# Optimization experiments

Hardware: AMD Instinct MI355X
Metric: run time of the kernel (lower is better)

The kernel has to match this reference:

```python
import jax, jax.numpy as jnp
import numpy as np

B, N, D, M, H = 8, 576, 512, 16, 8
DH = D // H
K = int(D * 0.1)  # sparsity_ratio=0.1 -> k=51
EPS = 1e-5


def setup_inputs() -> dict:
    key = jax.random.key(0)
    ks = jax.random.split(key, 12)
    s = 0.02
    return {
        "F_clean": jax.random.normal(ks[0], (B, N, D), jnp.float32),
        "in_proj_w": jax.random.normal(ks[1], (3 * D, D), jnp.float32) * s,
        "in_proj_b": jnp.zeros((3 * D,), jnp.float32),
        "out_proj_w": jax.random.normal(ks[2], (D, D), jnp.float32) * s,
        "out_proj_b": jnp.zeros((D,), jnp.float32),
        "w1": jax.random.normal(ks[3], (D, D), jnp.float32) * s,
        "b1": jnp.zeros((D,), jnp.float32),
        "ln_g": jnp.ones((D,), jnp.float32),
        "ln_b": jnp.zeros((D,), jnp.float32),
        "w2": jax.random.normal(ks[4], (M, D), jnp.float32) * s,
        "b2": jnp.zeros((M,), jnp.float32),
        "templates": jax.random.normal(ks[5], (M, D), jnp.float32),
    }


def reference(F_clean, in_proj_w, in_proj_b, out_proj_w, out_proj_b,
              w1, b1, ln_g, ln_b, w2, b2, templates):
    # --- self attention (torch MultiheadAttention, batch_first, eval mode) ---
    qkv = F_clean @ in_proj_w.T + in_proj_b              # [B,N,3D]
    q, k_, v = jnp.split(qkv, 3, axis=-1)
    def heads(t):
        return t.reshape(B, N, H, DH).transpose(0, 2, 1, 3)  # [B,H,N,dh]
    q, k_, v = heads(q), heads(k_), heads(v)
    scores = jnp.einsum('bhqd,bhkd->bhqk', q, k_) / jnp.sqrt(jnp.float32(DH))
    attn = jax.nn.softmax(scores, axis=-1)
    o = jnp.einsum('bhqk,bhkd->bhqd', attn, v).transpose(0, 2, 1, 3).reshape(B, N, D)
    attn_out = o @ out_proj_w.T + out_proj_b

    F_enh = F_clean + attn_out

    # --- decompose_mlp: Linear -> LayerNorm -> GELU(exact) -> Linear ---
    h = F_enh @ w1.T + b1
    mu = jnp.mean(h, axis=-1, keepdims=True)
    var = jnp.var(h, axis=-1, keepdims=True)
    h = (h - mu) / jnp.sqrt(var + EPS) * ln_g + ln_b
    h = jax.nn.gelu(h, approximate=False)
    components = h @ w2.T + b2                           # [B,N,M]

    # --- outer product: Q[b,n,d,m] = F[b,n,d] * templates[m,d] * comp[b,n,m] ---
    Q = F_clean[:, :, :, None] * templates.T[None, None, :, :] * components[:, :, None, :]

    # --- top-k sparsify along D for each (b,n,m) row ---
    Qr = Q.transpose(0, 1, 3, 2).reshape(B * N * M, D)
    _, topk_idx = jax.lax.top_k(jnp.abs(Qr), K)
    rows = jnp.arange(B * N * M)[:, None]
    mask = jnp.zeros_like(Qr).at[rows, topk_idx].set(1.0)
    Q_sparse = (Qr * mask).reshape(B, N, M, D).transpose(0, 1, 3, 2)
    return Q_sparse
```

## Files before the change

kernel.cpp:

```cpp
#include <hip/hip_runtime.h>
#include <math.h>

#define NNB   576
#define BNR   4608
#define KSEL  51

typedef unsigned short u16;
typedef __attribute__((ext_vector_type(8))) short bf16x8;
typedef __attribute__((ext_vector_type(4))) float f32x4;

__device__ __forceinline__ u16 f2bf(float f) {
    unsigned u = __float_as_uint(f);
    return (u16)((u + 0x8000u) >> 16);
}
__device__ __forceinline__ unsigned pack2(float a, float b) {
    unsigned ua = __float_as_uint(a), ub = __float_as_uint(b);
    return ((ua + 0x8000u) >> 16) | ((ub + 0x8000u) & 0xffff0000u);
}
__device__ __forceinline__ void load_lds16(const void* gp, void* lp) {
    __builtin_amdgcn_global_load_lds((const __attribute__((address_space(1))) void*)gp,
                                     (__attribute__((address_space(3))) void*)lp, 16, 0, 0);
}

__global__ __launch_bounds__(256)
void cast_bf16(const float* __restrict__ F, const float* __restrict__ ipw,
               const float* __restrict__ opw, const float* __restrict__ w1,
               u16* __restrict__ Fb, u16* __restrict__ ipwb,
               u16* __restrict__ opwb, u16* __restrict__ w1b)
{
    size_t i4 = ((size_t)blockIdx.x * 256 + threadIdx.x) * 4;
    const float* src; u16* dst; size_t off;
    if      (i4 < 2359296) { src = F;   dst = Fb;   off = i4; }
    else if (i4 < 3145728) { src = ipw; dst = ipwb; off = i4 - 2359296; }
    else if (i4 < 3407872) { src = opw; dst = opwb; off = i4 - 3145728; }
    else                   { src = w1;  dst = w1b;  off = i4 - 3407872; }
    float4 v = *(const float4*)(src + off);
    uint2 o; o.x = pack2(v.x, v.y); o.y = pack2(v.z, v.w);
    *(uint2*)(dst + off) = o;
}

template<bool RESID, bool OUT_BF16, bool QSCALE>
__global__ __launch_bounds__(256)
void gemm_mfma(const u16* __restrict__ A, const u16* __restrict__ Bw,
               const float* __restrict__ bias, const float* __restrict__ res,
               void* __restrict__ Cv, int Mr, int Nc, int Kd)
{
    __shared__ uint4 As4[1024];
    __shared__ uint4 Bs4[1024];
    const int tid = threadIdx.x;
    const int lane = tid & 63, w = tid >> 6;
    const int wu = __builtin_amdgcn_readfirstlane(w);
    const int r16 = lane & 15, quad = lane >> 4;
    const int wy = w >> 1, wx = w & 1;
    const int r0 = blockIdx.y << 7, c0 = blockIdx.x << 7;

    const u16* pA[4]; const u16* pB[4];
    #pragma unroll
    for (int rd = 0; rd < 4; ++rd) {
        const int c = (rd << 8) + tid;
        const int kb = c >> 9, g = (c >> 6) & 7, rr = (c >> 2) & 15, q = c & 3;
        const int row = (g << 4) + rr;
        const int koff = (kb << 5) + (q << 3);
        pA[rd] = A  + (size_t)(r0 + row) * Kd + koff;
        pB[rd] = Bw + (size_t)(c0 + row) * Kd + koff;
    }

    f32x4 acc[4][4];
    #pragma unroll
    for (int i = 0; i < 4; ++i)
        #pragma unroll
        for (int j = 0; j < 4; ++j) acc[i][j] = (f32x4){0.f, 0.f, 0.f, 0.f};

    for (int kk = 0; kk < Kd; kk += 64) {
        __syncthreads();
        #pragma unroll
        for (int rd = 0; rd < 4; ++rd) {
            load_lds16(pA[rd] + kk, (void*)(As4 + (rd << 8) + (wu << 6)));
            load_lds16(pB[rd] + kk, (void*)(Bs4 + (rd << 8) + (wu << 6)));
        }
        __syncthreads();
        #pragma unroll
        for (int kb = 0; kb < 2; ++kb) {
            bf16x8 af[4], bfr[4];
            #pragma unroll
            for (int i = 0; i < 4; ++i)
                af[i] = *(const bf16x8*)&As4[((kb * 8 + (wy << 2) + i) << 6) + (r16 << 2) + quad];
            #pragma unroll
            for (int j = 0; j < 4; ++j)
                bfr[j] = *(const bf16x8*)&Bs4[((kb * 8 + (wx << 2) + j) << 6) + (r16 << 2) + quad];
            #pragma unroll
            for (int i = 0; i < 4; ++i)
                #pragma unroll
                for (int j = 0; j < 4; ++j)
                    acc[i][j] = __builtin_amdgcn_mfma_f32_16x16x32_bf16(af[i], bfr[j], acc[i][j], 0, 0, 0);
        }
    }

    float bcol[4]; float scl[4];
    #pragma unroll
    for (int j = 0; j < 4; ++j) {
        const int col = c0 + (wx << 6) + (j << 4) + r16;
        bcol[j] = bias[col];
        scl[j] = (QSCALE && col < 512) ? 0.180336880111120426f : 1.0f;
    }
    #pragma unroll
    for (int i = 0; i < 4; ++i) {
        #pragma unroll
        for (int reg = 0; reg < 4; ++reg) {
            const int row = r0 + (wy << 6) + (i << 4) + (quad << 2) + reg;
            const size_t base = (size_t)row * Nc;
            #pragma unroll
            for (int j = 0; j < 4; ++j) {
                const int col = c0 + (wx << 6) + (j << 4) + r16;
                float v = acc[i][j][reg] + bcol[j];
                if (RESID) v += res[base + col];
                if (QSCALE) v *= scl[j];
                if (OUT_BF16) ((u16*)Cv)[base + col] = f2bf(v);
                else          ((float*)Cv)[base + col] = v;
            }
        }
    }
}

template<bool RESID, bool OUT_BF16>
__global__ __launch_bounds__(256)
void gemm_mfma64(const u16* __restrict__ A, const u16* __restrict__ Bw,
                 const float* __restrict__ bias, const float* __restrict__ res,
                 void* __restrict__ Cv, int Mr, int Nc, int Kd)
{
    __shared__ uint4 As4[512];
    __shared__ uint4 Bs4[1024];
    const int tid = threadIdx.x;
    const int lane = tid & 63, w = tid >> 6;
    const int wu = __builtin_amdgcn_readfirstlane(w);
    const int r16 = lane & 15, quad = lane >> 4;
    const int r0 = blockIdx.y << 6, c0 = blockIdx.x << 7;

    const u16* pA[2]; const u16* pB[4];
    #pragma unroll
    for (int rd = 0; rd < 2; ++rd) {
        const int c = (rd << 8) + tid;
        const int kb = c >> 8, g = (c >> 6) & 3, rr = (c >> 2) & 15, q = c & 3;
        pA[rd] = A + (size_t)(r0 + (g << 4) + rr) * Kd + (kb << 5) + (q << 3);
    }
    #pragma unroll
    for (int rd = 0; rd < 4; ++rd) {
        const int c = (rd << 8) + tid;
        const int kb = c >> 9, g = (c >> 6) & 7, rr = (c >> 2) & 15, q = c & 3;
        pB[rd] = Bw + (size_t)(c0 + (g << 4) + rr) * Kd + (kb << 5) + (q << 3);
    }

    f32x4 acc[4][2];
    #pragma unroll
    for (int i = 0; i < 4; ++i)
        #pragma unroll
        for (int j = 0; j < 2; ++j) acc[i][j] = (f32x4){0.f, 0.f, 0.f, 0.f};

    for (int kk = 0; kk < Kd; kk += 64) {
        __syncthreads();
        #pragma unroll
        for (int rd = 0; rd < 2; ++rd)
            load_lds16(pA[rd] + kk, (void*)(As4 + (rd << 8) + (wu << 6)));
        #pragma unroll
        for (int rd = 0; rd < 4; ++rd)
            load_lds16(pB[rd] + kk, (void*)(Bs4 + (rd << 8) + (wu << 6)));
        __syncthreads();
        #pragma unroll
        for (int kb = 0; kb < 2; ++kb) {
            bf16x8 af[4], bfr[2];
            #pragma unroll
            for (int i = 0; i < 4; ++i)
                af[i] = *(const bf16x8*)&As4[((kb * 4 + i) << 6) + (r16 << 2) + quad];
            #pragma unroll
            for (int j = 0; j < 2; ++j)
                bfr[j] = *(const bf16x8*)&Bs4[((kb * 8 + (w << 1) + j) << 6) + (r16 << 2) + quad];
            #pragma unroll
            for (int i = 0; i < 4; ++i)
                #pragma unroll
                for (int j = 0; j < 2; ++j)
                    acc[i][j] = __builtin_amdgcn_mfma_f32_16x16x32_bf16(af[i], bfr[j], acc[i][j], 0, 0, 0);
        }
    }

    float bcol[2];
    #pragma unroll
    for (int j = 0; j < 2; ++j) bcol[j] = bias[c0 + (w << 5) + (j << 4) + r16];
    #pragma unroll
    for (int i = 0; i < 4; ++i) {
        #pragma unroll
        for (int reg = 0; reg < 4; ++reg) {
            const int row = r0 + (i << 4) + (quad << 2) + reg;
            const size_t base = (size_t)row * Nc;
            #pragma unroll
            for (int j = 0; j < 2; ++j) {
                const int col = c0 + (w << 5) + (j << 4) + r16;
                float v = acc[i][j][reg] + bcol[j];
                if (RESID) v += res[base + col];
                if (OUT_BF16) ((u16*)Cv)[base + col] = f2bf(v);
                else          ((float*)Cv)[base + col] = v;
            }
        }
    }
}

__global__ __launch_bounds__(256)
void attn_mfma(const u16* __restrict__ qkv, u16* __restrict__ obuf)
{
    __shared__ uint4 Qf[512];
    __shared__ uint4 Kf[512];
    __shared__ u16  Vfs[4096];
    __shared__ u16  Pfs[4096];
    const int tid = threadIdx.x;
    const int lane = tid & 63, w = tid >> 6;
    const int wu = __builtin_amdgcn_readfirstlane(w);
    const int r16 = lane & 15, quad = lane >> 4;
    const int b = blockIdx.y >> 3, h = blockIdx.y & 7;
    const int i0 = blockIdx.x << 6;
    const u16* qb = qkv + (size_t)b * NNB * 1536 + h * 64;

    #pragma unroll
    for (int s = 0; s < 2; ++s) {
        const int linear = (s << 8) + tid;
        const int r = linear >> 3, q7 = linear & 7;
        uint4 v = *(const uint4*)(qb + (size_t)(i0 + r) * 1536 + (q7 << 3));
        Qf[(((q7 >> 2) * 4 + (r >> 4)) << 6) + ((r & 15) << 2) + (q7 & 3)] = v;
    }
    const u16* pK[2];
    #pragma unroll
    for (int rd = 0; rd < 2; ++rd) {
        const int c = (rd << 8) + tid;
        const int kb = c >> 8, g = (c >> 6) & 3, rr = (c >> 2) & 15, q = c & 3;
        pK[rd] = qb + 512 + (size_t)((g << 4) + rr) * 1536 + (kb << 5) + (q << 3);
    }

    float l_i[4] = {0.f, 0.f, 0.f, 0.f};
    f32x4 accO[4];
    #pragma unroll
    for (int f = 0; f < 4; ++f) accO[f] = (f32x4){0.f, 0.f, 0.f, 0.f};

    for (int j0 = 0; j0 < NNB; j0 += 64) {
        uint4 vR[2];
        #pragma unroll
        for (int s = 0; s < 2; ++s) {
            const int linear = (s << 8) + tid;
            const int r = linear >> 3, q7 = linear & 7;
            vR[s] = *(const uint4*)(qb + 1024 + (size_t)(j0 + r) * 1536 + (q7 << 3));
        }
        __syncthreads();
        load_lds16(pK[0] + (size_t)j0 * 1536, (void*)(Kf + (wu << 6)));
        load_lds16(pK[1] + (size_t)j0 * 1536, (void*)(Kf + 256 + (wu << 6)));
        #pragma unroll
        for (int s = 0; s < 2; ++s) {
            const int linear = (s << 8) + tid;
            const int r = linear >> 3, q7 = linear & 7;
            const u16* pe = (const u16*)&vR[s];
            const int jlow = r & 7, jq = (r >> 3) & 3, jkb = r >> 5;
            #pragma unroll
            for (int e = 0; e < 8; ++e) {
                const int d = (q7 << 3) + e;
                const int g = d >> 4;
                const int ch = ((jkb * 4 + g) << 6) + ((((d & 15) << 2) + jq) ^ g);
                Vfs[(ch << 3) + jlow] = pe[e];
            }
        }
        __syncthreads();

        f32x4 accS[4];
        #pragma unroll
        for (int f = 0; f < 4; ++f) accS[f] = (f32x4){0.f, 0.f, 0.f, 0.f};
        #pragma unroll
        for (int kb = 0; kb < 2; ++kb) {
            bf16x8 aq = *(const bf16x8*)&Qf[((kb * 4 + w) << 6) + (r16 << 2) + quad];
            #pragma unroll
            for (int f = 0; f < 4; ++f) {
                bf16x8 bk = *(const bf16x8*)&Kf[((kb * 4 + f) << 6) + (r16 << 2) + quad];
                accS[f] = __builtin_amdgcn_mfma_f32_16x16x32_bf16(aq, bk, accS[f], 0, 0, 0);
            }
        }
        #pragma unroll
        for (int reg = 0; reg < 4; ++reg) {
            const float s0 = exp2f(accS[0][reg]);
            const float s1 = exp2f(accS[1][reg]);
            const float s2 = exp2f(accS[2][reg]);
            const float s3 = exp2f(accS[3][reg]);
            l_i[reg] += (s0 + s1) + (s2 + s3);
            const int m = (quad << 2) + reg;
            const int sm = ((m & 3) << 2) + (m >> 2);
            const float pv[4] = {s0, s1, s2, s3};
            #pragma unroll
            for (int f = 0; f < 4; ++f) {
                const int k = (f << 4) + r16;
                const int ch = (((k >> 5) * 4 + w) << 6) + (((k >> 3) & 3) << 4) + sm;
                Pfs[(ch << 3) + (k & 7)] = f2bf(pv[f]);
            }
        }
        #pragma unroll
        for (int kb = 0; kb < 2; ++kb) {
            bf16x8 ap = *(const bf16x8*)&Pfs[((((kb * 4 + w) << 6) + (quad << 4) + ((r16 & 3) << 2) + (r16 >> 2)) << 3)];
            #pragma unroll
            for (int f = 0; f < 4; ++f) {
                bf16x8 bv = *(const bf16x8*)&Vfs[((((kb * 4 + f) << 6) + (((r16 << 2) + quad) ^ f)) << 3)];
                accO[f] = __builtin_amdgcn_mfma_f32_16x16x32_bf16(ap, bv, accO[f], 0, 0, 0);
            }
        }
    }
    #pragma unroll
    for (int reg = 0; reg < 4; ++reg) {
        float l = l_i[reg];
        l += __shfl_xor(l, 1); l += __shfl_xor(l, 2);
        l += __shfl_xor(l, 4); l += __shfl_xor(l, 8);
        const float inv = 1.0f / l;
        const size_t row = (size_t)(b * NNB + i0 + (w << 4) + (quad << 2) + reg);
        #pragma unroll
        for (int f = 0; f < 4; ++f)
            obuf[row * 512 + (h << 6) + (f << 4) + r16] = f2bf(accO[f][reg] * inv);
    }
}

__global__ __launch_bounds__(256)
void outer_topk(const float* __restrict__ F, const float* __restrict__ hraw,
                const float* __restrict__ lng, const float* __restrict__ lnb,
                const float* __restrict__ w2, const float* __restrict__ b2,
                const float* __restrict__ T, float* __restrict__ out)
{
    const int bn = blockIdx.x;
    const int tid = threadIdx.x;
    const int lane = tid & 63, w = tid >> 6;
    __shared__ float Fr[512];
    __shared__ float Hr[512];
    __shared__ unsigned keyslots[4][4][64];
    __shared__ float redsm[8];

    if (tid < 128)
        *(float4*)&Fr[tid << 2] = *(const float4*)(F + (size_t)bn * 512 + (tid << 2));
    const float* hp = hraw + (size_t)bn * 512;
    float x0 = hp[tid], x1 = hp[tid + 256];
    float s = x0 + x1, sq = x0 * x0 + x1 * x1;
    #pragma unroll
    for (int off = 32; off; off >>= 1) { s += __shfl_xor(s, off); sq += __shfl_xor(sq, off); }
    if (lane == 0) { redsm[w] = s; redsm[4 + w] = sq; }
    __syncthreads();
    s  = redsm[0] + redsm[1] + redsm[2] + redsm[3];
    sq = redsm[4] + redsm[5] + redsm[6] + redsm[7];
    const float mean = s * (1.0f / 512.0f);
    const float var  = sq * (1.0f / 512.0f) - mean * mean;
    const float rstd = rsqrtf(var + 1e-5f);
    float y = (x0 - mean) * rstd * lng[tid] + lnb[tid];
    Hr[tid] = 0.5f * y * (1.0f + erff(y * 0.70710678118654752f));
    y = (x1 - mean) * rstd * lng[tid + 256] + lnb[tid + 256];
    Hr[tid + 256] = 0.5f * y * (1.0f + erff(y * 0.70710678118654752f));
    __syncthreads();

    const int m0 = w << 2;
    float cm[4];
    #pragma unroll
    for (int mi = 0; mi < 4; ++mi) {
        const float* w2p = w2 + (size_t)(m0 + mi) * 512;
        float p = 0.f;
        #pragma unroll
        for (int t = 0; t < 8; ++t) p += Hr[lane + (t << 6)] * w2p[lane + (t << 6)];
        #pragma unroll
        for (int off = 32; off; off >>= 1) p += __shfl_xor(p, off);
        cm[mi] = p + b2[m0 + mi];
    }

    unsigned u[4][8]; unsigned smask[4];
    #pragma unroll
    for (int mi = 0; mi < 4; ++mi) {
        smask[mi] = 0u;
        const float* Tp = T + (size_t)(m0 + mi) * 512;
        #pragma unroll
        for (int t = 0; t < 8; ++t) {
            float pp = Fr[lane + (t << 6)] * Tp[lane + (t << 6)];
            float pc = pp * cm[mi];
            const unsigned bits = __float_as_uint(pc);
            u[mi][t] = bits & 0x7fffffffu;
            smask[mi] |= (bits >> 31) << t;
        }
    }

    unsigned pref[4] = {0u, 0u, 0u, 0u};
    int cntP[4] = {512, 512, 512, 512};
    int U[4] = {0, 0, 0, 0};
    for (int bit = 30; bit >= 23; --bit) {
        const unsigned msk = 1u << bit;
        #pragma unroll
        for (int mi = 0; mi < 4; ++mi) {
            const unsigned cand = pref[mi] | msk;
            int cnt = 0;
            #pragma unroll
            for (int t = 0; t < 8; ++t) cnt += __popcll(__ballot(u[mi][t] >= cand));
            if (cnt >= KSEL) { pref[mi] = cand; cntP[mi] = cnt; } else { U[mi] = cnt; }
        }
    }
    int blo[4];
    #pragma unroll
    for (int mi = 0; mi < 4; ++mi) {
        int b = 23;
        while ((cntP[mi] - U[mi]) > 64 && b > 0) {
            --b;
            const unsigned cand = pref[mi] | (1u << b);
            int cnt = 0;
            #pragma unroll
            for (int t = 0; t < 8; ++t) cnt += __popcll(__ballot(u[mi][t] >= cand));
            if (cnt >= KSEL) { pref[mi] = cand; cntP[mi] = cnt; } else { U[mi] = cnt; }
        }
        blo[mi] = b;
    }
    int need[4]; bool done[4];
    #pragma unroll
    for (int mi = 0; mi < 4; ++mi) {
        need[mi] = KSEL - U[mi];
        done[mi] = (need[mi] == cntP[mi] - U[mi]);
    }

    const unsigned long long lmask = (1ull << lane) - 1ull;
    unsigned kv[4] = {0u, 0u, 0u, 0u};
    #pragma unroll
    for (int mi = 0; mi < 4; ++mi) {
        if (done[mi]) continue;
        keyslots[w][mi][lane] = 0u;
        const int bl = blo[mi];
        const unsigned lowmask = (1u << bl) - 1u;
        int running = 0;
        #pragma unroll
        for (int t = 0; t < 8; ++t) {
            const bool tie = ((u[mi][t] ^ pref[mi]) >> bl) == 0u;
            const unsigned long long M = __ballot(tie);
            const int slot = running + __popcll(M & lmask);
            if (tie && slot < 64) {
                const unsigned key = ((u[mi][t] & lowmask) << 9) | (unsigned)(511 - ((t << 6) + lane));
                keyslots[w][mi][slot] = key;
            }
            running += __popcll(M);
        }
        kv[mi] = keyslots[w][mi][lane];
    }

    unsigned prefk[4] = {0u, 0u, 0u, 0u};
    for (int bb = 31; bb >= 0; --bb) {
        if (done[0] & done[1] & done[2] & done[3]) break;
        #pragma unroll
        for (int mi = 0; mi < 4; ++mi) {
            if (done[mi]) continue;
            const unsigned candk = prefk[mi] | (1u << bb);
            const int c = __popcll(__ballot(kv[mi] >= candk));
            if (c >= need[mi]) {
                prefk[mi] = candk;
                if (c == need[mi]) done[mi] = true;
            }
        }
    }

    float* ob = out + (size_t)bn * 8192 + m0;
    #pragma unroll
    for (int t = 0; t < 8; ++t) {
        const int d = (t << 6) + lane;
        float4 v;
        float* vv = &v.x;
        #pragma unroll
        for (int mi = 0; mi < 4; ++mi) {
            const unsigned uu = u[mi][t];
            const int bl = blo[mi];
            const bool tie = ((uu ^ pref[mi]) >> bl) == 0u;
            const unsigned key = ((uu & ((1u << bl) - 1u)) << 9) | (unsigned)(511 - d);
            const bool sel = (uu >= pref[mi] + (1u << bl)) || (tie && key >= prefk[mi]);
            const unsigned bits = uu | (((smask[mi] >> t) & 1u) << 31);
            vv[mi] = sel ? __uint_as_float(bits) : 0.0f;
        }
        *(float4*)(ob + (size_t)d * 16) = v;
    }
}

extern "C" void kernel_launch(void* const* d_in, const int* in_sizes, int n_in,
                              void* d_out, int out_size, void* d_ws, size_t ws_size,
                              hipStream_t stream)
{
    const float* F    = (const float*)d_in[0];
    const float* ipw  = (const float*)d_in[1];
    const float* ipb  = (const float*)d_in[2];
    const float* opw  = (const float*)d_in[3];
    const float* opb  = (const float*)d_in[4];
    const float* w1   = (const float*)d_in[5];
    const float* b1   = (const float*)d_in[6];
    const float* lng  = (const float*)d_in[7];
    const float* lnb  = (const float*)d_in[8];
    const float* w2   = (const float*)d_in[9];
    const float* b2   = (const float*)d_in[10];
    const float* tmpl = (const float*)d_in[11];

    char* wsb = (char*)d_ws;
    u16*   qkvb  = (u16*)wsb;
    u16*   obufb = (u16*)(wsb + 14155776);
    u16*   fenhb = (u16*)(wsb + 18874368);
    float* hbuf  = (float*)(wsb + 23592960);
    u16*   Fbf   = (u16*)(wsb + 33030144);
    u16*   ipwbf = (u16*)(wsb + 37748736);
    u16*   opwbf = (u16*)(wsb + 39321600);
    u16*   w1bf  = (u16*)(wsb + 39845888);

    cast_bf16<<<3584, 256, 0, stream>>>(F, ipw, opw, w1, Fbf, ipwbf, opwbf, w1bf);
    gemm_mfma<false, true, true><<<dim3(12, 36), 256, 0, stream>>>(Fbf, ipwbf, ipb, nullptr, qkvb, BNR, 1536, 512);
    attn_mfma<<<dim3(9, 64), 256, 0, stream>>>(qkvb, obufb);
    gemm_mfma64<true, true><<<dim3(4, 72), 256, 0, stream>>>(obufb, opwbf, opb, F, fenhb, BNR, 512, 512);
    gemm_mfma64<false, false><<<dim3(4, 72), 256, 0, stream>>>(fenhb, w1bf, b1, nullptr, hbuf, BNR, 512, 512);
    outer_topk<<<4608, 256, 0, stream>>>(F, hbuf, lng, lnb, w2, b2, tmpl, (float*)d_out);
}
```

Measured before the change: 296.0 us.

## Shrink GEMM tiles, pack V transposes, and use DPP reductions in top-k

The QKV projection moves from 128x128 to 64x128 tiles. The out-proj and w1 GEMMs use a new 64x64 tile kernel, which doubles the grid for better CU occupancy on the 4608-row problem. Attention V staging now loads two adjacent rows per thread and writes packed 32-bit pairs to LDS, halving LDS store count. In outer_topk, wavefront reductions switch from shfl_xor and ballot-popcount to DPP row and broadcast reductions, trading ballots for per-lane counts summed with DPP. Smaller tiles reduce operand reuse per block.

```diff
diff --git a/kernel.cpp b/kernel.cpp
--- a/kernel.cpp
+++ b/kernel.cpp
@@ -20,6 +20,24 @@
 __device__ __forceinline__ void load_lds16(const void* gp, void* lp) {
     __builtin_amdgcn_global_load_lds((const __attribute__((address_space(1))) void*)gp,
                                      (__attribute__((address_space(3))) void*)lp, 16, 0, 0);
+}
+__device__ __forceinline__ int dpp_red_add_i(int v) {
+    v += __builtin_amdgcn_update_dpp(0, v, 0x111, 0xf, 0xf, true);
+    v += __builtin_amdgcn_update_dpp(0, v, 0x112, 0xf, 0xf, true);
+    v += __builtin_amdgcn_update_dpp(0, v, 0x114, 0xf, 0xf, true);
+    v += __builtin_amdgcn_update_dpp(0, v, 0x118, 0xf, 0xf, true);
+    v += __builtin_amdgcn_update_dpp(0, v, 0x142, 0xa, 0xf, true);
+    v += __builtin_amdgcn_update_dpp(0, v, 0x143, 0xc, 0xf, true);
+    return __builtin_amdgcn_readlane(v, 63);
+}
+__device__ __forceinline__ float dpp_red_add_f(float x) {
+    x += __int_as_float(__builtin_amdgcn_update_dpp(0, __float_as_int(x), 0x111, 0xf, 0xf, true));
+    x += __int_as_float(__builtin_amdgcn_update_dpp(0, __float_as_int(x), 0x112, 0xf, 0xf, true));
+    x += __int_as_float(__builtin_amdgcn_update_dpp(0, __float_as_int(x), 0x114, 0xf, 0xf, true));
+    x += __int_as_float(__builtin_amdgcn_update_dpp(0, __float_as_int(x), 0x118, 0xf, 0xf, true));
+    x += __int_as_float(__builtin_amdgcn_update_dpp(0, __float_as_int(x), 0x142, 0xa, 0xf, true));
+    x += __int_as_float(__builtin_amdgcn_update_dpp(0, __float_as_int(x), 0x143, 0xc, 0xf, true));
+    return __int_as_float(__builtin_amdgcn_readlane(__float_as_int(x), 63));
 }
 
 __global__ __launch_bounds__(256)
@@ -41,89 +59,6 @@
 
 template<bool RESID, bool OUT_BF16, bool QSCALE>
 __global__ __launch_bounds__(256)
-void gemm_mfma(const u16* __restrict__ A, const u16* __restrict__ Bw,
-               const float* __restrict__ bias, const float* __restrict__ res,
-               void* __restrict__ Cv, int Mr, int Nc, int Kd)
-{
-    __shared__ uint4 As4[1024];
-    __shared__ uint4 Bs4[1024];
-    const int tid = threadIdx.x;
-    const int lane = tid & 63, w = tid >> 6;
-    const int wu = __builtin_amdgcn_readfirstlane(w);
-    const int r16 = lane & 15, quad = lane >> 4;
-    const int wy = w >> 1, wx = w & 1;
-    const int r0 = blockIdx.y << 7, c0 = blockIdx.x << 7;
-
-    const u16* pA[4]; const u16* pB[4];
-    #pragma unroll
-    for (int rd = 0; rd < 4; ++rd) {
-        const int c = (rd << 8) + tid;
-        const int kb = c >> 9, g = (c >> 6) & 7, rr = (c >> 2) & 15, q = c & 3;
-        const int row = (g << 4) + rr;
-        const int koff = (kb << 5) + (q << 3);
-        pA[rd] = A  + (size_t)(r0 + row) * Kd + koff;
-        pB[rd] = Bw + (size_t)(c0 + row) * Kd + koff;
-    }
-
-    f32x4 acc[4][4];
-    #pragma unroll
-    for (int i = 0; i < 4; ++i)
-        #pragma unroll
-        for (int j = 0; j < 4; ++j) acc[i][j] = (f32x4){0.f, 0.f, 0.f, 0.f};
-
-    for (int kk = 0; kk < Kd; kk += 64) {
-        __syncthreads();
-        #pragma unroll
-        for (int rd = 0; rd < 4; ++rd) {
-            load_lds16(pA[rd] + kk, (void*)(As4 + (rd << 8) + (wu << 6)));
-            load_lds16(pB[rd] + kk, (void*)(Bs4 + (rd << 8) + (wu << 6)));
-        }
-        __syncthreads();
-        #pragma unroll
-        for (int kb = 0; kb < 2; ++kb) {
-            bf16x8 af[4], bfr[4];
-            #pragma unroll
-            for (int i = 0; i < 4; ++i)
-                af[i] = *(const bf16x8*)&As4[((kb * 8 + (wy << 2) + i) << 6) + (r16 << 2) + quad];
-            #pragma unroll
-            for (int j = 0; j < 4; ++j)
-                bfr[j] = *(const bf16x8*)&Bs4[((kb * 8 + (wx << 2) + j) << 6) + (r16 << 2) + quad];
-            #pragma unroll
-            for (int i = 0; i < 4; ++i)
-                #pragma unroll
-                for (int j = 0; j < 4; ++j)
-                    acc[i][j] = __builtin_amdgcn_mfma_f32_16x16x32_bf16(af[i], bfr[j], acc[i][j], 0, 0, 0);
-        }
-    }
-
-    float bcol[4]; float scl[4];
-    #pragma unroll
-    for (int j = 0; j < 4; ++j) {
-        const int col = c0 + (wx << 6) + (j << 4) + r16;
-        bcol[j] = bias[col];
-        scl[j] = (QSCALE && col < 512) ? 0.180336880111120426f : 1.0f;
-    }
-    #pragma unroll
-    for (int i = 0; i < 4; ++i) {
-        #pragma unroll
-        for (int reg = 0; reg < 4; ++reg) {
-            const int row = r0 + (wy << 6) + (i << 4) + (quad << 2) + reg;
-            const size_t base = (size_t)row * Nc;
-            #pragma unroll
-            for (int j = 0; j < 4; ++j) {
-                const int col = c0 + (wx << 6) + (j << 4) + r16;
-                float v = acc[i][j][reg] + bcol[j];
-                if (RESID) v += res[base + col];
-                if (QSCALE) v *= scl[j];
-                if (OUT_BF16) ((u16*)Cv)[base + col] = f2bf(v);
-                else          ((float*)Cv)[base + col] = v;
-            }
-        }
-    }
-}
-
-template<bool RESID, bool OUT_BF16>
-__global__ __launch_bounds__(256)
 void gemm_mfma64(const u16* __restrict__ A, const u16* __restrict__ Bw,
                  const float* __restrict__ bias, const float* __restrict__ res,
                  void* __restrict__ Cv, int Mr, int Nc, int Kd)
@@ -182,9 +117,13 @@
         }
     }
 
-    float bcol[2];
-    #pragma unroll
-    for (int j = 0; j < 2; ++j) bcol[j] = bias[c0 + (w << 5) + (j << 4) + r16];
+    float bcol[2], scl[2];
+    #pragma unroll
+    for (int j = 0; j < 2; ++j) {
+        const int col = c0 + (w << 5) + (j << 4) + r16;
+        bcol[j] = bias[col];
+        scl[j] = (QSCALE && col < 512) ? 0.180336880111120426f : 1.0f;
+    }
     #pragma unroll
     for (int i = 0; i < 4; ++i) {
         #pragma unroll
@@ -194,6 +133,85 @@
             #pragma unroll
             for (int j = 0; j < 2; ++j) {
                 const int col = c0 + (w << 5) + (j << 4) + r16;
+                float v = acc[i][j][reg] + bcol[j];
+                if (RESID) v += res[base + col];
+                if (QSCALE) v *= scl[j];
+                if (OUT_BF16) ((u16*)Cv)[base + col] = f2bf(v);
+                else          ((float*)Cv)[base + col] = v;
+            }
+        }
+    }
+}
+
+template<bool RESID, bool OUT_BF16>
+__global__ __launch_bounds__(256)
+void gemm_6464(const u16* __restrict__ A, const u16* __restrict__ Bw,
+               const float* __restrict__ bias, const float* __restrict__ res,
+               void* __restrict__ Cv, int Mr, int Nc, int Kd)
+{
+    __shared__ uint4 As4[512];
+    __shared__ uint4 Bs4[512];
+    const int tid = threadIdx.x;
+    const int lane = tid & 63, w = tid >> 6;
+    const int wu = __builtin_amdgcn_readfirstlane(w);
+    const int r16 = lane & 15, quad = lane >> 4;
+    const int wy = w >> 1, wx = w & 1;
+    const int r0 = blockIdx.y << 6, c0 = blockIdx.x << 6;
+
+    const u16* pA[2]; const u16* pB[2];
+    #pragma unroll
+    for (int rd = 0; rd < 2; ++rd) {
+        const int c = (rd << 8) + tid;
+        const int kb = c >> 8, g = (c >> 6) & 3, rr = (c >> 2) & 15, q = c & 3;
+        const int row = (g << 4) + rr;
+        const int koff = (kb << 5) + (q << 3);
+        pA[rd] = A  + (size_t)(r0 + row) * Kd + koff;
+        pB[rd] = Bw + (size_t)(c0 + row) * Kd + koff;
+    }
+
+    f32x4 acc[2][2];
+    #pragma unroll
+    for (int i = 0; i < 2; ++i)
+        #pragma unroll
+        for (int j = 0; j < 2; ++j) acc[i][j] = (f32x4){0.f, 0.f, 0.f, 0.f};
+
+    for (int kk = 0; kk < Kd; kk += 64) {
+        __syncthreads();
+        #pragma unroll
+        for (int rd = 0; rd < 2; ++rd) {
+            load_lds16(pA[rd] + kk, (void*)(As4 + (rd << 8) + (wu << 6)));
+            load_lds16(pB[rd] + kk, (void*)(Bs4 + (rd << 8) + (wu << 6)));
+        }
+        __syncthreads();
+        #pragma unroll
+        for (int kb = 0; kb < 2; ++kb) {
+            bf16x8 af[2], bfr[2];
+            #pragma unroll
+            for (int i = 0; i < 2; ++i)
+                af[i] = *(const bf16x8*)&As4[((kb * 4 + (wy << 1) + i) << 6) + (r16 << 2) + quad];
+            #pragma unroll
+            for (int j = 0; j < 2; ++j)
+                bfr[j] = *(const bf16x8*)&Bs4[((kb * 4 + (wx << 1) + j) << 6) + (r16 << 2) + quad];
+            #pragma unroll
+            for (int i = 0; i < 2; ++i)
+                #pragma unroll
+                for (int j = 0; j < 2; ++j)
+                    acc[i][j] = __builtin_amdgcn_mfma_f32_16x16x32_bf16(af[i], bfr[j], acc[i][j], 0, 0, 0);
+        }
+    }
+
+    float bcol[2];
+    #pragma unroll
+    for (int j = 0; j < 2; ++j) bcol[j] = bias[c0 + (wx << 5) + (j << 4) + r16];
+    #pragma unroll
+    for (int i = 0; i < 2; ++i) {
+        #pragma unroll
+        for (int reg = 0; reg < 4; ++reg) {
+            const int row = r0 + (wy << 5) + (i << 4) + (quad << 2) + reg;
+            const size_t base = (size_t)row * Nc;
+            #pragma unroll
+            for (int j = 0; j < 2; ++j) {
+                const int col = c0 + (wx << 5) + (j << 4) + r16;
                 float v = acc[i][j][reg] + bcol[j];
                 if (RESID) v += res[base + col];
                 if (OUT_BF16) ((u16*)Cv)[base + col] = f2bf(v);
@@ -232,6 +250,9 @@
         const int kb = c >> 8, g = (c >> 6) & 3, rr = (c >> 2) & 15, q = c & 3;
         pK[rd] = qb + 512 + (size_t)((g << 4) + rr) * 1536 + (kb << 5) + (q << 3);
     }
+    const int vp = tid >> 3, vq7 = tid & 7;
+    const int vj = vp << 1;
+    const int vjl2 = (vj & 7) >> 1, vjq = (vj >> 3) & 3, vjkb = vj >> 5;
 
     float l_i[4] = {0.f, 0.f, 0.f, 0.f};
     f32x4 accO[4];
@@ -239,28 +260,22 @@
     for (int f = 0; f < 4; ++f) accO[f] = (f32x4){0.f, 0.f, 0.f, 0.f};
 
     for (int j0 = 0; j0 < NNB; j0 += 64) {
-        uint4 vR[2];
-        #pragma unroll
-        for (int s = 0; s < 2; ++s) {
-            const int linear = (s << 8) + tid;
-            const int r = linear >> 3, q7 = linear & 7;
-            vR[s] = *(const uint4*)(qb + 1024 + (size_t)(j0 + r) * 1536 + (q7 << 3));
-        }
+        const u16* vbase = qb + 1024 + (size_t)(j0 + vj) * 1536 + (vq7 << 3);
+        uint4 vA = *(const uint4*)vbase;
+        uint4 vB = *(const uint4*)(vbase + 1536);
         __syncthreads();
         load_lds16(pK[0] + (size_t)j0 * 1536, (void*)(Kf + (wu << 6)));
         load_lds16(pK[1] + (size_t)j0 * 1536, (void*)(Kf + 256 + (wu << 6)));
-        #pragma unroll
-        for (int s = 0; s < 2; ++s) {
-            const int linear = (s << 8) + tid;
-            const int r = linear >> 3, q7 = linear & 7;
-            const u16* pe = (const u16*)&vR[s];
-            const int jlow = r & 7, jq = (r >> 3) & 3, jkb = r >> 5;
+        {
+            const u16* ea = (const u16*)&vA;
+            const u16* eb = (const u16*)&vB;
+            unsigned* V32 = (unsigned*)Vfs;
             #pragma unroll
             for (int e = 0; e < 8; ++e) {
-                const int d = (q7 << 3) + e;
+                const int d = (vq7 << 3) + e;
                 const int g = d >> 4;
-                const int ch = ((jkb * 4 + g) << 6) + ((((d & 15) << 2) + jq) ^ g);
-                Vfs[(ch << 3) + jlow] = pe[e];
+                const int ch = ((vjkb * 4 + g) << 6) + ((((d & 15) << 2) + vjq) ^ g);
+                V32[(ch << 2) + vjl2] = (unsigned)ea[e] | ((unsigned)eb[e] << 16);
             }
         }
         __syncthreads();
@@ -335,13 +350,12 @@
         *(float4*)&Fr[tid << 2] = *(const float4*)(F + (size_t)bn * 512 + (tid << 2));
     const float* hp = hraw + (size_t)bn * 512;
     float x0 = hp[tid], x1 = hp[tid + 256];
-    float s = x0 + x1, sq = x0 * x0 + x1 * x1;
-    #pragma unroll
-    for (int off = 32; off; off >>= 1) { s += __shfl_xor(s, off); sq += __shfl_xor(sq, off); }
-    if (lane == 0) { redsm[w] = s; redsm[4 + w] = sq; }
+    float sw = dpp_red_add_f(x0 + x1);
+    float sqw = dpp_red_add_f(x0 * x0 + x1 * x1);
+    if (lane == 0) { redsm[w] = sw; redsm[4 + w] = sqw; }
     __syncthreads();
-    s  = redsm[0] + redsm[1] + redsm[2] + redsm[3];
-    sq = redsm[4] + redsm[5] + redsm[6] + redsm[7];
+    const float s  = redsm[0] + redsm[1] + redsm[2] + redsm[3];
+    const float sq = redsm[4] + redsm[5] + redsm[6] + redsm[7];
     const float mean = s * (1.0f / 512.0f);
     const float var  = sq * (1.0f / 512.0f) - mean * mean;
     const float rstd = rsqrtf(var + 1e-5f);
@@ -359,9 +373,7 @@
         float p = 0.f;
         #pragma unroll
         for (int t = 0; t < 8; ++t) p += Hr[lane + (t << 6)] * w2p[lane + (t << 6)];
-        #pragma unroll
-        for (int off = 32; off; off >>= 1) p += __shfl_xor(p, off);
-        cm[mi] = p + b2[m0 + mi];
+        cm[mi] = dpp_red_add_f(p) + b2[m0 + mi];
     }
 
     unsigned u[4][8]; unsigned smask[4];
@@ -384,13 +396,22 @@
     int U[4] = {0, 0, 0, 0};
     for (int bit = 30; bit >= 23; --bit) {
         const unsigned msk = 1u << bit;
+        unsigned cand[4]; int cl[4];
         #pragma unroll
         for (int mi = 0; mi < 4; ++mi) {
-            const unsigned cand = pref[mi] | msk;
-            int cnt = 0;
-            #pragma unroll
-            for (int t = 0; t < 8; ++t) cnt += __popcll(__ballot(u[mi][t] >= cand));
-            if (cnt >= KSEL) { pref[mi] = cand; cntP[mi] = cnt; } else { U[mi] = cnt; }
+            cand[mi] = pref[mi] | msk;
+            int cc = 0;
+            #pragma unroll
+            for (int t = 0; t < 8; ++t) cc += (u[mi][t] >= cand[mi]) ? 1 : 0;
+            cl[mi] = cc;
+        }
+        int cnt[4];
+        #pragma unroll
+        for (int mi = 0; mi < 4; ++mi) cnt[mi] = dpp_red_add_i(cl[mi]);
+        #pragma unroll
+        for (int mi = 0; mi < 4; ++mi) {
+            if (cnt[mi] >= KSEL) { pref[mi] = cand[mi]; cntP[mi] = cnt[mi]; }
+            else U[mi] = cnt[mi];
         }
     }
     int blo[4];
@@ -400,10 +421,11 @@
         while ((cntP[mi] - U[mi]) > 64 && b > 0) {
             --b;
             const unsigned cand = pref[mi] | (1u << b);
-            int cnt = 0;
-            #pragma unroll
-            for (int t = 0; t < 8; ++t) cnt += __popcll(__ballot(u[mi][t] >= cand));
-            if (cnt >= KSEL) { pref[mi] = cand; cntP[mi] = cnt; } else { U[mi] = cnt; }
+            int cc = 0;
+            #pragma unroll
+            for (int t = 0; t < 8; ++t) cc += (u[mi][t] >= cand) ? 1 : 0;
+            const int cnt = dpp_red_add_i(cc);
+            if (cnt >= KSEL) { pref[mi] = cand; cntP[mi] = cnt; } else U[mi] = cnt;
         }
         blo[mi] = b;
     }
@@ -500,9 +522,9 @@
     u16*   w1bf  = (u16*)(wsb + 39845888);
 
     cast_bf16<<<3584, 256, 0, stream>>>(F, ipw, opw, w1, Fbf, ipwbf, opwbf, w1bf);
-    gemm_mfma<false, true, true><<<dim3(12, 36), 256, 0, stream>>>(Fbf, ipwbf, ipb, nullptr, qkvb, BNR, 1536, 512);
+    gemm_mfma64<false, true, true><<<dim3(12, 72), 256, 0, stream>>>(Fbf, ipwbf, ipb, nullptr, qkvb, BNR, 1536, 512);
     attn_mfma<<<dim3(9, 64), 256, 0, stream>>>(qkvb, obufb);
-    gemm_mfma64<true, true><<<dim3(4, 72), 256, 0, stream>>>(obufb, opwbf, opb, F, fenhb, BNR, 512, 512);
-    gemm_mfma64<false, false><<<dim3(4, 72), 256, 0, stream>>>(fenhb, w1bf, b1, nullptr, hbuf, BNR, 512, 512);
+    gemm_6464<true, true><<<dim3(8, 72), 256, 0, stream>>>(obufb, opwbf, opb, F, fenhb, BNR, 512, 512);
+    gemm_6464<false, false><<<dim3(8, 72), 256, 0, stream>>>(fenhb, w1bf, b1, nullptr, hbuf, BNR, 512, 512);
     outer_topk<<<4608, 256, 0, stream>>>(F, hbuf, lng, lnb, w2, b2, tmpl, (float*)d_out);
 }
```

Result: faster. 290.2 us (-2.0%).
